# Kernel tuning notes

Hardware: AMD Instinct MI355X
Metric: run time of the kernel (lower is better)

Reference implementation:

```python
import jax, jax.numpy as jnp
import numpy as np

ATT_HEADS = 4
H_FEATS = 16
IN_FEATS = 64
N_NODES = 50000
N_EDGES = 1000000


def setup_inputs() -> dict:
    key = jax.random.key(0)
    ks = jax.random.split(key, 12)
    h = jax.random.normal(ks[0], (N_NODES, IN_FEATS), dtype=jnp.float32)
    src_idx = jax.random.randint(ks[1], (N_EDGES,), 0, N_NODES)
    dst_idx = jax.random.randint(ks[2], (N_EDGES,), 0, N_NODES)
    s = 1.0 / np.sqrt(IN_FEATS)
    # w_liner: Linear(in_feats, h_feats*att_heads)
    W_w = jax.random.uniform(ks[3], (IN_FEATS, H_FEATS * ATT_HEADS), jnp.float32, -s, s)
    b_w = jax.random.uniform(ks[4], (H_FEATS * ATT_HEADS,), jnp.float32, -s, s)
    # atten: Linear(2*h_feats, 1)
    sa = 1.0 / np.sqrt(2 * H_FEATS)
    W_a = jax.random.uniform(ks[5], (2 * H_FEATS, 1), jnp.float32, -sa, sa)
    b_a = jax.random.uniform(ks[6], (1,), jnp.float32, -sa, sa)
    # relation_aware: d_liner Linear(in_feats, in_feats), f_liner Linear(3*in_feats, 1)
    W_d = jax.random.uniform(ks[7], (IN_FEATS, IN_FEATS), jnp.float32, -s, s)
    b_d = jax.random.uniform(ks[8], (IN_FEATS,), jnp.float32, -s, s)
    sf = 1.0 / np.sqrt(3 * IN_FEATS)
    W_f = jax.random.uniform(ks[9], (3 * IN_FEATS, 1), jnp.float32, -sf, sf)
    b_f = jax.random.uniform(ks[10], (1,), jnp.float32, -sf, sf)
    return {"h": h, "src_idx": src_idx, "dst_idx": dst_idx,
            "W_w": W_w, "b_w": b_w, "W_a": W_a, "b_a": b_a,
            "W_d": W_d, "b_d": b_d, "W_f": W_f, "b_f": b_f}


def reference(h, src_idx, dst_idx, W_w, b_w, W_a, b_a, W_d, b_d, W_f, b_f):
    N = h.shape[0]
    # sign_edges: relation_aware score -> sign per edge
    s_feat = h[src_idx] @ W_d + b_d            # [E, F]
    d_feat = h[dst_idx] @ W_d + b_d            # [E, F]
    e_feat = jnp.concatenate([s_feat, d_feat, s_feat - d_feat], axis=-1)
    score = jnp.tanh(e_feat @ W_f + b_f)[:, 0]  # [E]
    sign = jnp.sign(score)
    # node transform
    hp = h @ W_w + b_w                          # [N, H*hf]
    # message: signed src features, per-head concat with dst, attention logit
    sf = (sign[:, None] * hp[src_idx]).reshape(-1, ATT_HEADS, H_FEATS)  # [E,H,hf]
    df = hp[dst_idx].reshape(-1, ATT_HEADS, H_FEATS)                    # [E,H,hf]
    z = jnp.concatenate([sf, df], axis=-1)                              # [E,H,2hf]
    alpha = jax.nn.leaky_relu(z @ W_a + b_a)                            # [E,H,1]
    # reduce: segment softmax over incoming edges of each dst node
    amax = jax.ops.segment_max(alpha, dst_idx, num_segments=N)          # [N,H,1]
    ex = jnp.exp(alpha - amax[dst_idx])
    esum = jax.ops.segment_sum(ex, dst_idx, num_segments=N)             # [N,H,1]
    w = ex / esum[dst_idx]                                              # [E,H,1]
    out = jax.ops.segment_sum(w * sf, dst_idx, num_segments=N)          # [N,H,hf]
    return out.reshape(N, ATT_HEADS * H_FEATS)
```

## Files before the change

### kernel.cpp

```cpp
#include <hip/hip_runtime.h>
#include <hip/hip_fp16.h>

constexpr int F  = 64;
constexpr int HEADS = 4;
constexpr int SHARDS = 8;
constexpr int CAPS = 16;
constexpr int MAXDEG = 64;

__global__ __launch_bounds__(256) void node_wd_kernel(
    const float* __restrict__ h,
    const float* __restrict__ W_d, const float* __restrict__ b_d,
    const float* __restrict__ W_f,
    float* __restrict__ tfeat,
    float* __restrict__ u_arr, float* __restrict__ v_arr,
    unsigned* __restrict__ cnt, unsigned* __restrict__ of_cnt, int N)
{
    __shared__ float sWT[F * F];
    __shared__ float sb[F];
    __shared__ double swfA[F], swfB[F];

    int tid = threadIdx.x;
    for (int i = tid; i < F * F; i += 256) {
        int k = i >> 6, j = i & 63;
        sWT[j * F + k] = W_d[i];
    }
    if (tid < F) {
        sb[tid] = b_d[tid];
        swfA[tid] = (double)W_f[tid] + (double)W_f[2 * F + tid];
        swfB[tid] = (double)W_f[F + tid] - (double)W_f[2 * F + tid];
    }
    if (blockIdx.x == 0 && tid == 0) *of_cnt = 0;
    __syncthreads();

    int n = blockIdx.x * 256 + tid;
    if (n >= N) return;

#pragma unroll
    for (int x = 0; x < SHARDS; x++) cnt[(size_t)x * N + n] = 0;

    float4 hv[16];
    const float4* h4 = reinterpret_cast<const float4*>(h + (size_t)n * F);
#pragma unroll
    for (int i = 0; i < 16; i++) hv[i] = h4[i];

    double u = 0.0, v = 0.0;
    float4 tq;
    float4* trow = reinterpret_cast<float4*>(tfeat + (size_t)n * F);
#pragma unroll 4
    for (int j = 0; j < F; j++) {
        const float4* row = reinterpret_cast<const float4*>(&sWT[j * F]);
        float t = 0.f;
#pragma unroll
        for (int kk = 0; kk < 16; kk++) {
            float4 w = row[kk];
            float4 x = hv[kk];
            t = fmaf(x.x, w.x, t);
            t = fmaf(x.y, w.y, t);
            t = fmaf(x.z, w.z, t);
            t = fmaf(x.w, w.w, t);
        }
        t = t + sb[j];
        u = fma((double)t, swfA[j], u);
        v = fma((double)t, swfB[j], v);
        if ((j & 3) == 0) tq.x = t;
        else if ((j & 3) == 1) tq.y = t;
        else if ((j & 3) == 2) tq.z = t;
        else { tq.w = t; trow[j >> 2] = tq; }
    }
    u_arr[n] = (float)u;
    v_arr[n] = (float)v;
}

__device__ __noinline__ float tier2_sign(
    const float* __restrict__ tfeat, const float* __restrict__ sWf,
    int s, int d, float bf)
{
    const float4* ts = reinterpret_cast<const float4*>(tfeat + (size_t)s * F);
    const float4* td = reinterpret_cast<const float4*>(tfeat + (size_t)d * F);
    float sv[F];
#pragma unroll
    for (int i = 0; i < 16; i++) {
        float4 a = ts[i];
        sv[4 * i + 0] = a.x; sv[4 * i + 1] = a.y;
        sv[4 * i + 2] = a.z; sv[4 * i + 3] = a.w;
    }
    float acc = 0.f;
#pragma unroll
    for (int j = 0; j < F; j++) acc = fmaf(sv[j], sWf[j], acc);
#pragma unroll
    for (int i = 0; i < 16; i++) {
        float4 a = td[i];
        acc = fmaf(a.x, sWf[F + 4 * i + 0], acc);
        acc = fmaf(a.y, sWf[F + 4 * i + 1], acc);
        acc = fmaf(a.z, sWf[F + 4 * i + 2], acc);
        acc = fmaf(a.w, sWf[F + 4 * i + 3], acc);
    }
#pragma unroll
    for (int i = 0; i < 16; i++) {
        float4 a = td[i];
        acc = fmaf(sv[4 * i + 0] - a.x, sWf[2 * F + 4 * i + 0], acc);
        acc = fmaf(sv[4 * i + 1] - a.y, sWf[2 * F + 4 * i + 1], acc);
        acc = fmaf(sv[4 * i + 2] - a.z, sWf[2 * F + 4 * i + 2], acc);
        acc = fmaf(sv[4 * i + 3] - a.w, sWf[2 * F + 4 * i + 3], acc);
    }
    float sp = acc + bf;
    return (sp > 0.f) ? 1.f : (sp < 0.f ? -1.f : 0.f);
}

__global__ __launch_bounds__(256) void ww_count_scatter_kernel(
    const float* __restrict__ h,
    const float* __restrict__ W_w, const float* __restrict__ b_w,
    const float* __restrict__ W_a,
    __half* __restrict__ hp,
    float* __restrict__ a_src, float* __restrict__ a_dst,
    const int* __restrict__ src_idx, const int* __restrict__ dst_idx,
    const float* __restrict__ u_arr, const float* __restrict__ v_arr,
    const float* __restrict__ tfeat, const float* __restrict__ W_f,
    const float* __restrict__ b_f,
    unsigned* __restrict__ cnt, unsigned* __restrict__ slot,
    unsigned* __restrict__ of_list, unsigned* __restrict__ of_cnt,
    int N, int E, int nbw, unsigned of_cap)
{
    __shared__ float sWT[F * F];
    __shared__ float sb[F];
    __shared__ float sWa[32];

    int tid = threadIdx.x;

    if (blockIdx.x < nbw) {
        for (int i = tid; i < F * F; i += 256) {
            int k = i >> 6, j = i & 63;
            sWT[j * F + k] = W_w[i];
        }
        if (tid < F) sb[tid] = b_w[tid];
        if (tid < 32) sWa[tid] = W_a[tid];
        __syncthreads();

        int n = blockIdx.x * 256 + tid;
        if (n >= N) return;

        float4 hv[16];
        const float4* h4 = reinterpret_cast<const float4*>(h + (size_t)n * F);
#pragma unroll
        for (int i = 0; i < 16; i++) hv[i] = h4[i];

        __half2* prow = reinterpret_cast<__half2*>(hp + (size_t)n * F);
#pragma unroll
        for (int qh = 0; qh < 4; qh++) {
            float asq = 0.f, adq = 0.f;
            float pprev = 0.f;
#pragma unroll 4
            for (int jj = 0; jj < 16; jj++) {
                int j = qh * 16 + jj;
                const float4* row = reinterpret_cast<const float4*>(&sWT[j * F]);
                float p = 0.f;
#pragma unroll
                for (int kk = 0; kk < 16; kk++) {
                    float4 w = row[kk];
                    float4 x = hv[kk];
                    p = fmaf(x.x, w.x, p);
                    p = fmaf(x.y, w.y, p);
                    p = fmaf(x.z, w.z, p);
                    p = fmaf(x.w, w.w, p);
                }
                p = p + sb[j];
                asq = fmaf(p, sWa[jj], asq);
                adq = fmaf(p, sWa[16 + jj], adq);
                if ((jj & 1) == 0) pprev = p;
                else prow[j >> 1] = __floats2half2_rn(pprev, p);
            }
            a_src[n * HEADS + qh] = asq;
            a_dst[n * HEADS + qh] = adq;
        }
        return;
    }

    float* sWf = sWT;
    if (tid < 3 * F) sWf[tid] = W_f[tid];
    __syncthreads();

    unsigned xcc;
    asm volatile("s_getreg_b32 %0, hwreg(HW_REG_XCC_ID)" : "=s"(xcc));
    xcc &= (SHARDS - 1);

    float bf = b_f[0];
    int eb = blockIdx.x - nbw;
    int e0 = eb * 512 + tid;
    int e1 = e0 + 256;
    bool ok0 = e0 < E, ok1 = e1 < E;

    int s0 = 0, d0 = 0, s1 = 0, d1 = 0;
    if (ok0) { s0 = src_idx[e0]; d0 = dst_idx[e0]; }
    if (ok1) { s1 = src_idx[e1]; d1 = dst_idx[e1]; }

    float us0 = ok0 ? u_arr[s0] : 0.f, vd0 = ok0 ? v_arr[d0] : 0.f;
    float us1 = ok1 ? u_arr[s1] : 0.f, vd1 = ok1 ? v_arr[d1] : 0.f;
    unsigned p0 = ok0 ? __hip_atomic_fetch_add(&cnt[(size_t)xcc * N + d0], 1u,
                          __ATOMIC_RELAXED, __HIP_MEMORY_SCOPE_WORKGROUP) : 0u;
    unsigned p1 = ok1 ? __hip_atomic_fetch_add(&cnt[(size_t)xcc * N + d1], 1u,
                          __ATOMIC_RELAXED, __HIP_MEMORY_SCOPE_WORKGROUP) : 0u;

    float m0 = us0 + vd0 + bf;
    float m1 = us1 + vd1 + bf;

    float sg0 = (fabsf(m0) >= 1e-4f) ? ((m0 > 0.f) ? 1.f : -1.f)
                                     : (ok0 ? tier2_sign(tfeat, sWf, s0, d0, bf) : 0.f);
    float sg1 = (fabsf(m1) >= 1e-4f) ? ((m1 > 0.f) ? 1.f : -1.f)
                                     : (ok1 ? tier2_sign(tfeat, sWf, s1, d1, bf) : 0.f);

    if (ok0) {
        unsigned c0 = (sg0 > 0.f) ? 0u : (sg0 < 0.f ? 1u : 2u);
        unsigned val = (unsigned)s0 | (c0 << 30);
        if (p0 < (unsigned)CAPS) slot[((size_t)xcc * N + d0) * CAPS + p0] = val;
        else {
            unsigned oi = atomicAdd(of_cnt, 1u);
            if (oi < of_cap) { of_list[2 * oi] = (unsigned)d0; of_list[2 * oi + 1] = val; }
        }
    }
    if (ok1) {
        unsigned c1 = (sg1 > 0.f) ? 0u : (sg1 < 0.f ? 1u : 2u);
        unsigned val = (unsigned)s1 | (c1 << 30);
        if (p1 < (unsigned)CAPS) slot[((size_t)xcc * N + d1) * CAPS + p1] = val;
        else {
            unsigned oi = atomicAdd(of_cnt, 1u);
            if (oi < of_cap) { of_list[2 * oi] = (unsigned)d1; of_list[2 * oi + 1] = val; }
        }
    }
}

__global__ __launch_bounds__(256) void dst_gather_kernel(
    const unsigned* __restrict__ cnt,
    const unsigned* __restrict__ slot,
    const unsigned* __restrict__ of_list, const unsigned* __restrict__ of_cnt,
    const float* __restrict__ a_src, const float* __restrict__ a_dst,
    const float* __restrict__ b_a,
    const __half* __restrict__ hp,
    float* __restrict__ out, int N)
{
    __shared__ float sw[4][MAXDEG * 4];
    __shared__ unsigned ssrc[4][MAXDEG];

    int tid = threadIdx.x;
    int wslot = tid >> 6;
    int lane = tid & 63;
    int q = lane >> 4;
    int d = (blockIdx.x * 256 + tid) >> 6;
    bool valid = d < N;

    float ba = b_a[0];
    float4 ad4 = make_float4(0.f, 0.f, 0.f, 0.f);
    unsigned csh[SHARDS], pre[SHARDS];
    unsigned deg = 0;
    bool ofl = false;
    if (valid) {
        ad4 = *reinterpret_cast<const float4*>(a_dst + (size_t)d * HEADS);
#pragma unroll
        for (int x = 0; x < SHARDS; x++) {
            unsigned c = cnt[(size_t)x * N + d];
            csh[x] = c; pre[x] = deg; deg += c;
            if (c > (unsigned)CAPS) ofl = true;
        }
    }
    float adq = (q == 0) ? ad4.x : (q == 1) ? ad4.y : (q == 2) ? ad4.z : ad4.w;
    bool fast = valid && (deg <= (unsigned)MAXDEG) && !ofl;

    float4 p = make_float4(0.f, 0.f, 0.f, 0.f);
    if (fast && lane < (int)deg) {
        int shard = 0; unsigned pos = 0;
#pragma unroll
        for (int x = 0; x < SHARDS; x++)
            if ((unsigned)lane >= pre[x] && (unsigned)lane < pre[x] + csh[x]) {
                shard = x; pos = (unsigned)lane - pre[x];
            }
        unsigned sp = slot[((size_t)shard * N + d) * CAPS + pos];
        unsigned s = sp & 0x3FFFFFFFu;
        unsigned c = sp >> 30;
        float sgn = (c == 0u) ? 1.f : (c == 1u ? -1.f : 0.f);
        float4 as4 = *reinterpret_cast<const float4*>(a_src + (size_t)s * HEADS);
        float ap0 = fmaf(sgn, as4.x, ad4.x) + ba;
        float ap1 = fmaf(sgn, as4.y, ad4.y) + ba;
        float ap2 = fmaf(sgn, as4.z, ad4.z) + ba;
        float ap3 = fmaf(sgn, as4.w, ad4.w) + ba;
        float e0 = expf(ap0 > 0.f ? ap0 : 0.01f * ap0);
        float e1 = expf(ap1 > 0.f ? ap1 : 0.01f * ap1);
        float e2 = expf(ap2 > 0.f ? ap2 : 0.01f * ap2);
        float e3 = expf(ap3 > 0.f ? ap3 : 0.01f * ap3);
        p = make_float4(e0, e1, e2, e3);
        *reinterpret_cast<float4*>(&sw[wslot][lane * 4]) =
            make_float4(sgn * e0, sgn * e1, sgn * e2, sgn * e3);
        ssrc[wslot][lane] = s;
    }
    if (valid && !fast) {
        for (int x = 0; x < SHARDS; x++) {
            unsigned cc = min(csh[x], (unsigned)CAPS);
            for (unsigned i = lane; i < cc; i += 64) {
                unsigned sp = slot[((size_t)x * N + d) * CAPS + i];
                unsigned s = sp & 0x3FFFFFFFu;
                unsigned c = sp >> 30;
                float sgn = (c == 0u) ? 1.f : (c == 1u ? -1.f : 0.f);
                float4 as4 = *reinterpret_cast<const float4*>(a_src + (size_t)s * HEADS);
                float ap0 = fmaf(sgn, as4.x, ad4.x) + ba;
                float ap1 = fmaf(sgn, as4.y, ad4.y) + ba;
                float ap2 = fmaf(sgn, as4.z, ad4.z) + ba;
                float ap3 = fmaf(sgn, as4.w, ad4.w) + ba;
                p.x += expf(ap0 > 0.f ? ap0 : 0.01f * ap0);
                p.y += expf(ap1 > 0.f ? ap1 : 0.01f * ap1);
                p.z += expf(ap2 > 0.f ? ap2 : 0.01f * ap2);
                p.w += expf(ap3 > 0.f ? ap3 : 0.01f * ap3);
            }
        }
        unsigned on = *of_cnt;
        for (unsigned i = lane; i < on; i += 64) {
            if (of_list[2 * i] == (unsigned)d) {
                unsigned sp = of_list[2 * i + 1];
                unsigned s = sp & 0x3FFFFFFFu;
                unsigned c = sp >> 30;
                float sgn = (c == 0u) ? 1.f : (c == 1u ? -1.f : 0.f);
                float4 as4 = *reinterpret_cast<const float4*>(a_src + (size_t)s * HEADS);
                float ap0 = fmaf(sgn, as4.x, ad4.x) + ba;
                float ap1 = fmaf(sgn, as4.y, ad4.y) + ba;
                float ap2 = fmaf(sgn, as4.z, ad4.z) + ba;
                float ap3 = fmaf(sgn, as4.w, ad4.w) + ba;
                p.x += expf(ap0 > 0.f ? ap0 : 0.01f * ap0);
                p.y += expf(ap1 > 0.f ? ap1 : 0.01f * ap1);
                p.z += expf(ap2 > 0.f ? ap2 : 0.01f * ap2);
                p.w += expf(ap3 > 0.f ? ap3 : 0.01f * ap3);
            }
        }
    }
    __syncthreads();

#pragma unroll
    for (int off = 32; off >= 1; off >>= 1) {
        p.x += __shfl_xor(p.x, off);
        p.y += __shfl_xor(p.y, off);
        p.z += __shfl_xor(p.z, off);
        p.w += __shfl_xor(p.w, off);
    }
    if (!valid) return;

    float esq = (q == 0) ? p.x : (q == 1) ? p.y : (q == 2) ? p.z : p.w;
    float rinv = (deg > 0) ? (1.0f / esq) : 0.f;

    float a0 = 0.f, a1 = 0.f, a2 = 0.f, a3 = 0.f;
    if (fast) {
        const float* swb = &sw[wslot][0];
        const unsigned* ssb = &ssrc[wslot][0];
        unsigned t0 = 0;
        for (; t0 + 8 <= deg; t0 += 8) {
            float w0 = swb[(t0 + 0) * 4 + q], w1 = swb[(t0 + 1) * 4 + q];
            float w2 = swb[(t0 + 2) * 4 + q], w3 = swb[(t0 + 3) * 4 + q];
            float w4 = swb[(t0 + 4) * 4 + q], w5 = swb[(t0 + 5) * 4 + q];
            float w6 = swb[(t0 + 6) * 4 + q], w7 = swb[(t0 + 7) * 4 + q];
            unsigned s0 = ssb[t0 + 0], s1 = ssb[t0 + 1];
            unsigned s2 = ssb[t0 + 2], s3 = ssb[t0 + 3];
            unsigned s4 = ssb[t0 + 4], s5 = ssb[t0 + 5];
            unsigned s6 = ssb[t0 + 6], s7 = ssb[t0 + 7];
            float h0 = __half2float(hp[((size_t)s0 << 6) | (unsigned)lane]);
            float h1 = __half2float(hp[((size_t)s1 << 6) | (unsigned)lane]);
            float h2 = __half2float(hp[((size_t)s2 << 6) | (unsigned)lane]);
            float h3 = __half2float(hp[((size_t)s3 << 6) | (unsigned)lane]);
            float h4 = __half2float(hp[((size_t)s4 << 6) | (unsigned)lane]);
            float h5 = __half2float(hp[((size_t)s5 << 6) | (unsigned)lane]);
            float h6 = __half2float(hp[((size_t)s6 << 6) | (unsigned)lane]);
            float h7 = __half2float(hp[((size_t)s7 << 6) | (unsigned)lane]);
            a0 = fmaf(w0, h0, a0); a1 = fmaf(w1, h1, a1);
            a2 = fmaf(w2, h2, a2); a3 = fmaf(w3, h3, a3);
            a0 = fmaf(w4, h4, a0); a1 = fmaf(w5, h5, a1);
            a2 = fmaf(w6, h6, a2); a3 = fmaf(w7, h7, a3);
        }
        for (; t0 < deg; t0++) {
            float w = swb[t0 * 4 + q];
            unsigned s = ssb[t0];
            a0 = fmaf(w, __half2float(hp[((size_t)s << 6) | (unsigned)lane]), a0);
        }
    } else {
        for (int x = 0; x < SHARDS; x++) {
            unsigned cc = min(csh[x], (unsigned)CAPS);
            for (unsigned i = 0; i < cc; i++) {
                unsigned sp = slot[((size_t)x * N + d) * CAPS + i];
                unsigned s = sp & 0x3FFFFFFFu;
                unsigned c = sp >> 30;
                float g = (c == 0u) ? 1.f : (c == 1u ? -1.f : 0.f);
                float asv = a_src[s * HEADS + q];
                float ap = fmaf(g, asv, adq) + ba;
                float ev = expf(ap > 0.f ? ap : 0.01f * ap);
                a0 = fmaf(ev * g, __half2float(hp[((size_t)s << 6) | (unsigned)lane]), a0);
            }
        }
        unsigned on = *of_cnt;
        for (unsigned i = 0; i < on; i++) {
            if (of_list[2 * i] == (unsigned)d) {
                unsigned sp = of_list[2 * i + 1];
                unsigned s = sp & 0x3FFFFFFFu;
                unsigned c = sp >> 30;
                float g = (c == 0u) ? 1.f : (c == 1u ? -1.f : 0.f);
                float asv = a_src[s * HEADS + q];
                float ap = fmaf(g, asv, adq) + ba;
                float ev = expf(ap > 0.f ? ap : 0.01f * ap);
                a0 = fmaf(ev * g, __half2float(hp[((size_t)s << 6) | (unsigned)lane]), a0);
            }
        }
    }
    out[((size_t)d << 6) | (unsigned)lane] = ((a0 + a1) + (a2 + a3)) * rinv;
}

extern "C" void kernel_launch(void* const* d_in, const int* in_sizes, int n_in,
                              void* d_out, int out_size, void* d_ws, size_t ws_size,
                              hipStream_t stream)
{
    const float* h       = (const float*)d_in[0];
    const int*   src_idx = (const int*)d_in[1];
    const int*   dst_idx = (const int*)d_in[2];
    const float* W_w     = (const float*)d_in[3];
    const float* b_w     = (const float*)d_in[4];
    const float* W_a     = (const float*)d_in[5];
    const float* b_a     = (const float*)d_in[6];
    const float* W_d     = (const float*)d_in[7];
    const float* b_d     = (const float*)d_in[8];
    const float* W_f     = (const float*)d_in[9];
    const float* b_f     = (const float*)d_in[10];

    int N = in_sizes[0] / F;
    int E = in_sizes[1];
    int nb = (N + 255) / 256;
    int neb = (E + 511) / 512;
    unsigned of_cap = (unsigned)(E / 8);

    char* ws = (char*)d_ws;
    float*    tfeat  = (float*)ws;     ws += (size_t)N * F * 4;
    __half*   hp     = (__half*)ws;    ws += (size_t)N * F * 2;
    float*    u_arr  = (float*)ws;     ws += (size_t)N * 4;
    float*    v_arr  = (float*)ws;     ws += (size_t)N * 4;
    float*    a_src  = (float*)ws;     ws += (size_t)N * HEADS * 4;
    float*    a_dst  = (float*)ws;     ws += (size_t)N * HEADS * 4;
    unsigned* cnt    = (unsigned*)ws;  ws += (size_t)SHARDS * N * 4;
    unsigned* of_cnt = (unsigned*)ws;  ws += 64;
    unsigned* slot   = (unsigned*)ws;  ws += (size_t)SHARDS * N * CAPS * 4;
    unsigned* of_list= (unsigned*)ws;  ws += (size_t)of_cap * 8;

    float* out = (float*)d_out;

    node_wd_kernel<<<nb, 256, 0, stream>>>(
        h, W_d, b_d, W_f, tfeat, u_arr, v_arr, cnt, of_cnt, N);

    ww_count_scatter_kernel<<<nb + neb, 256, 0, stream>>>(
        h, W_w, b_w, W_a, hp, a_src, a_dst,
        src_idx, dst_idx, u_arr, v_arr, tfeat, W_f, b_f,
        cnt, slot, of_list, of_cnt, N, E, nb, of_cap);

    dst_gather_kernel<<<(N * 64 + 255) / 256, 256, 0, stream>>>(
        cnt, slot, of_list, of_cnt, a_src, a_dst, b_a, hp, out, N);
}
```

Baseline: 130.1 us.

## Compress edge slot buckets to 16-bit indices with separate sign bytes

Splits each packed 32-bit edge slot into a 16-bit source index and an 8-bit sign code, and halves per-shard bucket capacity from 16 to 8. The aim is to shrink the bucket workspace and the scattered write and read traffic between the scatter and gather kernels. It also pads the transposed weight tile in LDS to a stride of 68 to avoid bank conflicts, and clamps the overflow count to its capacity. The trade-offs are that source indices now only fit when N is below 65536, and the smaller buckets send more edges through the slow linearly scanned overflow list.

```diff
diff --git a/kernel.cpp b/kernel.cpp
--- a/kernel.cpp
+++ b/kernel.cpp
@@ -4,8 +4,9 @@
 constexpr int F  = 64;
 constexpr int HEADS = 4;
 constexpr int SHARDS = 8;
-constexpr int CAPS = 16;
+constexpr int CAPS = 8;
 constexpr int MAXDEG = 64;
+constexpr int WSTR = 68;
 
 __global__ __launch_bounds__(256) void node_wd_kernel(
     const float* __restrict__ h,
@@ -15,14 +16,14 @@
     float* __restrict__ u_arr, float* __restrict__ v_arr,
     unsigned* __restrict__ cnt, unsigned* __restrict__ of_cnt, int N)
 {
-    __shared__ float sWT[F * F];
+    __shared__ float sWT[F * WSTR];
     __shared__ float sb[F];
     __shared__ double swfA[F], swfB[F];
 
     int tid = threadIdx.x;
     for (int i = tid; i < F * F; i += 256) {
         int k = i >> 6, j = i & 63;
-        sWT[j * F + k] = W_d[i];
+        sWT[j * WSTR + k] = W_d[i];
     }
     if (tid < F) {
         sb[tid] = b_d[tid];
@@ -48,7 +49,7 @@
     float4* trow = reinterpret_cast<float4*>(tfeat + (size_t)n * F);
 #pragma unroll 4
     for (int j = 0; j < F; j++) {
-        const float4* row = reinterpret_cast<const float4*>(&sWT[j * F]);
+        const float4* row = reinterpret_cast<const float4*>(&sWT[j * WSTR]);
         float t = 0.f;
 #pragma unroll
         for (int kk = 0; kk < 16; kk++) {
@@ -117,11 +118,12 @@
     const float* __restrict__ u_arr, const float* __restrict__ v_arr,
     const float* __restrict__ tfeat, const float* __restrict__ W_f,
     const float* __restrict__ b_f,
-    unsigned* __restrict__ cnt, unsigned* __restrict__ slot,
+    unsigned* __restrict__ cnt,
+    unsigned short* __restrict__ slot16, unsigned char* __restrict__ sgn8,
     unsigned* __restrict__ of_list, unsigned* __restrict__ of_cnt,
     int N, int E, int nbw, unsigned of_cap)
 {
-    __shared__ float sWT[F * F];
+    __shared__ float sWT[F * WSTR];
     __shared__ float sb[F];
     __shared__ float sWa[32];
 
@@ -130,7 +132,7 @@
     if (blockIdx.x < nbw) {
         for (int i = tid; i < F * F; i += 256) {
             int k = i >> 6, j = i & 63;
-            sWT[j * F + k] = W_w[i];
+            sWT[j * WSTR + k] = W_w[i];
         }
         if (tid < F) sb[tid] = b_w[tid];
         if (tid < 32) sWa[tid] = W_a[tid];
@@ -152,7 +154,7 @@
 #pragma unroll 4
             for (int jj = 0; jj < 16; jj++) {
                 int j = qh * 16 + jj;
-                const float4* row = reinterpret_cast<const float4*>(&sWT[j * F]);
+                const float4* row = reinterpret_cast<const float4*>(&sWT[j * WSTR]);
                 float p = 0.f;
 #pragma unroll
                 for (int kk = 0; kk < 16; kk++) {
@@ -210,32 +212,36 @@
 
     if (ok0) {
         unsigned c0 = (sg0 > 0.f) ? 0u : (sg0 < 0.f ? 1u : 2u);
-        unsigned val = (unsigned)s0 | (c0 << 30);
-        if (p0 < (unsigned)CAPS) slot[((size_t)xcc * N + d0) * CAPS + p0] = val;
-        else {
+        if (p0 < (unsigned)CAPS) {
+            size_t idx = ((size_t)xcc * N + d0) * CAPS + p0;
+            slot16[idx] = (unsigned short)s0;
+            sgn8[idx] = (unsigned char)c0;
+        } else {
             unsigned oi = atomicAdd(of_cnt, 1u);
-            if (oi < of_cap) { of_list[2 * oi] = (unsigned)d0; of_list[2 * oi + 1] = val; }
+            if (oi < of_cap) { of_list[2 * oi] = (unsigned)d0; of_list[2 * oi + 1] = (unsigned)s0 | (c0 << 30); }
         }
     }
     if (ok1) {
         unsigned c1 = (sg1 > 0.f) ? 0u : (sg1 < 0.f ? 1u : 2u);
-        unsigned val = (unsigned)s1 | (c1 << 30);
-        if (p1 < (unsigned)CAPS) slot[((size_t)xcc * N + d1) * CAPS + p1] = val;
-        else {
+        if (p1 < (unsigned)CAPS) {
+            size_t idx = ((size_t)xcc * N + d1) * CAPS + p1;
+            slot16[idx] = (unsigned short)s1;
+            sgn8[idx] = (unsigned char)c1;
+        } else {
             unsigned oi = atomicAdd(of_cnt, 1u);
-            if (oi < of_cap) { of_list[2 * oi] = (unsigned)d1; of_list[2 * oi + 1] = val; }
+            if (oi < of_cap) { of_list[2 * oi] = (unsigned)d1; of_list[2 * oi + 1] = (unsigned)s1 | (c1 << 30); }
         }
     }
 }
 
 __global__ __launch_bounds__(256) void dst_gather_kernel(
     const unsigned* __restrict__ cnt,
-    const unsigned* __restrict__ slot,
+    const unsigned short* __restrict__ slot16, const unsigned char* __restrict__ sgn8,
     const unsigned* __restrict__ of_list, const unsigned* __restrict__ of_cnt,
     const float* __restrict__ a_src, const float* __restrict__ a_dst,
     const float* __restrict__ b_a,
     const __half* __restrict__ hp,
-    float* __restrict__ out, int N)
+    float* __restrict__ out, int N, unsigned of_cap)
 {
     __shared__ float sw[4][MAXDEG * 4];
     __shared__ unsigned ssrc[4][MAXDEG];
@@ -272,9 +278,9 @@
             if ((unsigned)lane >= pre[x] && (unsigned)lane < pre[x] + csh[x]) {
                 shard = x; pos = (unsigned)lane - pre[x];
             }
-        unsigned sp = slot[((size_t)shard * N + d) * CAPS + pos];
-        unsigned s = sp & 0x3FFFFFFFu;
-        unsigned c = sp >> 30;
+        size_t idx = ((size_t)shard * N + d) * CAPS + pos;
+        unsigned s = slot16[idx];
+        unsigned c = sgn8[idx];
         float sgn = (c == 0u) ? 1.f : (c == 1u ? -1.f : 0.f);
         float4 as4 = *reinterpret_cast<const float4*>(a_src + (size_t)s * HEADS);
         float ap0 = fmaf(sgn, as4.x, ad4.x) + ba;
@@ -294,9 +300,9 @@
         for (int x = 0; x < SHARDS; x++) {
             unsigned cc = min(csh[x], (unsigned)CAPS);
             for (unsigned i = lane; i < cc; i += 64) {
-                unsigned sp = slot[((size_t)x * N + d) * CAPS + i];
-                unsigned s = sp & 0x3FFFFFFFu;
-                unsigned c = sp >> 30;
+                size_t idx = ((size_t)x * N + d) * CAPS + i;
+                unsigned s = slot16[idx];
+                unsigned c = sgn8[idx];
                 float sgn = (c == 0u) ? 1.f : (c == 1u ? -1.f : 0.f);
                 float4 as4 = *reinterpret_cast<const float4*>(a_src + (size_t)s * HEADS);
                 float ap0 = fmaf(sgn, as4.x, ad4.x) + ba;
@@ -309,7 +315,7 @@
                 p.w += expf(ap3 > 0.f ? ap3 : 0.01f * ap3);
             }
         }
-        unsigned on = *of_cnt;
+        unsigned on = min(*of_cnt, of_cap);
         for (unsigned i = lane; i < on; i += 64) {
             if (of_list[2 * i] == (unsigned)d) {
                 unsigned sp = of_list[2 * i + 1];
@@ -378,9 +384,9 @@
         for (int x = 0; x < SHARDS; x++) {
             unsigned cc = min(csh[x], (unsigned)CAPS);
             for (unsigned i = 0; i < cc; i++) {
-                unsigned sp = slot[((size_t)x * N + d) * CAPS + i];
-                unsigned s = sp & 0x3FFFFFFFu;
-                unsigned c = sp >> 30;
+                size_t idx = ((size_t)x * N + d) * CAPS + i;
+                unsigned s = slot16[idx];
+                unsigned c = sgn8[idx];
                 float g = (c == 0u) ? 1.f : (c == 1u ? -1.f : 0.f);
                 float asv = a_src[s * HEADS + q];
                 float ap = fmaf(g, asv, adq) + ba;
@@ -388,7 +394,7 @@
                 a0 = fmaf(ev * g, __half2float(hp[((size_t)s << 6) | (unsigned)lane]), a0);
             }
         }
-        unsigned on = *of_cnt;
+        unsigned on = min(*of_cnt, of_cap);
         for (unsigned i = 0; i < on; i++) {
             if (of_list[2 * i] == (unsigned)d) {
                 unsigned sp = of_list[2 * i + 1];
@@ -428,16 +434,17 @@
     unsigned of_cap = (unsigned)(E / 8);
 
     char* ws = (char*)d_ws;
-    float*    tfeat  = (float*)ws;     ws += (size_t)N * F * 4;
-    __half*   hp     = (__half*)ws;    ws += (size_t)N * F * 2;
-    float*    u_arr  = (float*)ws;     ws += (size_t)N * 4;
-    float*    v_arr  = (float*)ws;     ws += (size_t)N * 4;
-    float*    a_src  = (float*)ws;     ws += (size_t)N * HEADS * 4;
-    float*    a_dst  = (float*)ws;     ws += (size_t)N * HEADS * 4;
-    unsigned* cnt    = (unsigned*)ws;  ws += (size_t)SHARDS * N * 4;
-    unsigned* of_cnt = (unsigned*)ws;  ws += 64;
-    unsigned* slot   = (unsigned*)ws;  ws += (size_t)SHARDS * N * CAPS * 4;
-    unsigned* of_list= (unsigned*)ws;  ws += (size_t)of_cap * 8;
+    float*          tfeat  = (float*)ws;          ws += (size_t)N * F * 4;
+    __half*         hp     = (__half*)ws;         ws += (size_t)N * F * 2;
+    float*          u_arr  = (float*)ws;          ws += (size_t)N * 4;
+    float*          v_arr  = (float*)ws;          ws += (size_t)N * 4;
+    float*          a_src  = (float*)ws;          ws += (size_t)N * HEADS * 4;
+    float*          a_dst  = (float*)ws;          ws += (size_t)N * HEADS * 4;
+    unsigned*       cnt    = (unsigned*)ws;       ws += (size_t)SHARDS * N * 4;
+    unsigned*       of_cnt = (unsigned*)ws;       ws += 64;
+    unsigned short* slot16 = (unsigned short*)ws; ws += (size_t)SHARDS * N * CAPS * 2;
+    unsigned char*  sgn8   = (unsigned char*)ws;  ws += (size_t)SHARDS * N * CAPS;
+    unsigned*       of_list= (unsigned*)ws;       ws += (size_t)of_cap * 8;
 
     float* out = (float*)d_out;
 
@@ -447,8 +454,8 @@
     ww_count_scatter_kernel<<<nb + neb, 256, 0, stream>>>(
         h, W_w, b_w, W_a, hp, a_src, a_dst,
         src_idx, dst_idx, u_arr, v_arr, tfeat, W_f, b_f,
-        cnt, slot, of_list, of_cnt, N, E, nb, of_cap);
+        cnt, slot16, sgn8, of_list, of_cnt, N, E, nb, of_cap);
 
     dst_gather_kernel<<<(N * 64 + 255) / 256, 256, 0, stream>>>(
-        cnt, slot, of_list, of_cnt, a_src, a_dst, b_a, hp, out, N);
+        cnt, slot16, sgn8, of_list, of_cnt, a_src, a_dst, b_a, hp, out, N, of_cap);
 }
```

After: 185.1 us. +42.3%, slower.
